# Performance work log

Measured on AMD Instinct MI355X. Metric: run time of the kernel, lower is better.

Reference implementation:

```python
import jax, jax.numpy as jnp
import numpy as np

EMBED_DIM = 1024
NUM_HEADS = 16
HEAD_DIM = EMBED_DIM // NUM_HEADS
SCALE = HEAD_DIM ** -0.5


def setup_inputs() -> dict:
    key = jax.random.key(0)
    k_x, k_wqkv, k_bqkv, k_wo, k_bo = jax.random.split(key, 5)
    B, T, C = 2, 2048, EMBED_DIM
    bound = 1.0 / np.sqrt(C)
    return {
        "x": jax.random.normal(k_x, (B, T, C), dtype=jnp.float32),
        "w_qkv": jax.random.uniform(k_wqkv, (C, 3 * C), jnp.float32, -bound, bound),
        "b_qkv": jax.random.uniform(k_bqkv, (3 * C,), jnp.float32, -bound, bound),
        "w_out": jax.random.uniform(k_wo, (C, C), jnp.float32, -bound, bound),
        "b_out": jax.random.uniform(k_bo, (C,), jnp.float32, -bound, bound),
    }


def reference(x, w_qkv, b_qkv, w_out, b_out):
    B, T, C = x.shape
    H, D = NUM_HEADS, HEAD_DIM
    qkv = x @ w_qkv + b_qkv                      # [B,T,3C]
    q, k, v = jnp.split(qkv, 3, axis=-1)         # each [B,T,C]
    q = q.reshape(B, T, H, D).transpose(0, 2, 1, 3)  # [B,H,T,D]
    k = k.reshape(B, T, H, D).transpose(0, 2, 1, 3)
    v = v.reshape(B, T, H, D).transpose(0, 2, 1, 3)
    scores = jnp.einsum("bhqd,bhkd->bhqk", q, k) * SCALE  # [B,H,T,T]
    weights = jax.nn.softmax(scores, axis=-1)
    out = jnp.einsum("bhqk,bhkd->bhqd", weights, v)       # [B,H,T,D]
    concat = out.transpose(0, 2, 1, 3).reshape(B, T, C)
    return concat @ w_out + b_out
```

## Files before the change

kernel.cpp:

```cpp
#include <hip/hip_runtime.h>

typedef _Float16 f16;
typedef _Float16 f16x8 __attribute__((ext_vector_type(8)));
typedef _Float16 f16x4 __attribute__((ext_vector_type(4)));
typedef float f32x4 __attribute__((ext_vector_type(4)));
typedef float f32x16 __attribute__((ext_vector_type(16)));
typedef unsigned int u32x4 __attribute__((ext_vector_type(4)));

#define SCALE_Q (0.125f * 1.44269504088896f)

__device__ __forceinline__ f32x4 mfma16x16x32(f16x8 a, f16x8 b, f32x4 c) {
  return __builtin_amdgcn_mfma_f32_16x16x32_f16(a, b, c, 0, 0, 0);
}
__device__ __forceinline__ f32x16 mfma32x32x16(f16x8 a, f16x8 b, f32x16 c) {
  return __builtin_amdgcn_mfma_f32_32x32x16_f16(a, b, c, 0, 0, 0);
}

__device__ __forceinline__ float fexp2(float x) {
  return __builtin_amdgcn_exp2f(x);
}

typedef const __attribute__((address_space(1))) void* gptr1;
typedef __attribute__((address_space(3))) void* lptr3;
__device__ __forceinline__ void gload_lds16(const void* g, void* l) {
  __builtin_amdgcn_global_load_lds((gptr1)g, (lptr3)l, 16, 0, 0);
}

__device__ __forceinline__ unsigned pk2(float a, float b) {
  return __builtin_bit_cast(unsigned, __builtin_amdgcn_cvt_pkrtz(a, b));
}

__global__ __launch_bounds__(256)
void prep(const float* __restrict__ x, f16* __restrict__ xh,
          const float* __restrict__ w_qkv, f16* __restrict__ wqkvT,
          const float* __restrict__ w_out, f16* __restrict__ woutT) {
  __shared__ float tile[32][33];
  const int bid = blockIdx.x;
  const int tid = threadIdx.x;
  if (bid < 4096) {
    int i = bid * 256 + tid;
    float4 v = reinterpret_cast<const float4*>(x)[i];
    f16x4 o = {(f16)v.x, (f16)v.y, (f16)v.z, (f16)v.w};
    reinterpret_cast<f16x4*>(xh)[i] = o;
    return;
  }
  const float* in;
  f16* out;
  int bx, by, R, Cin;
  if (bid < 7168) {
    int t = bid - 4096;
    in = w_qkv; out = wqkvT; R = 1024; Cin = 3072;
    bx = (t % 96) * 32; by = (t / 96) * 32;
  } else {
    int t = bid - 7168;
    in = w_out; out = woutT; R = 1024; Cin = 1024;
    bx = (t % 32) * 32; by = (t / 32) * 32;
  }
  int tx = tid & 31, ty = tid >> 5;
#pragma unroll
  for (int i = ty; i < 32; i += 8)
    tile[i][tx] = in[(size_t)(by + i) * Cin + bx + tx];
  __syncthreads();
#pragma unroll
  for (int i = ty; i < 32; i += 8)
    out[(size_t)(bx + i) * R + by + tx] = (f16)tile[tx][i];
}

__global__ __launch_bounds__(256)
void gemm_qkv(const f16* __restrict__ A, const f16* __restrict__ Bt,
              const float* __restrict__ bias, f16* __restrict__ qQ,
              f16* __restrict__ kP, f16* __restrict__ vP) {
  constexpr int BM = 128, BN = 128, BK = 32, K = 1024;
  __shared__ f16 As[BM * BK];
  __shared__ f16 Bs[BN * BK];
  const int tid = threadIdx.x;
  const int l = tid & 63;
  const int w = tid >> 6;
  const int wr = w >> 1, wc = w & 1;
  const int bid = blockIdx.x;
  const int xcd = bid & 7, idx = bid >> 3;
  const int xg = xcd & 3, yg = xcd >> 2;
  const int mx = xg * 8 + (idx & 7);
  const int ny = yg * 12 + (idx >> 3);
  const int bm = mx * BM, bn = ny * BN;
  const int l15 = l & 15, lhi = l >> 4;

  f32x4 acc[4][4] = {};

  const char* Ab = (const char*)A;
  const char* Bb = (const char*)Bt;
  const size_t rowbytes = (size_t)K * 2;

  for (int kt = 0; kt < K; kt += BK) {
    __syncthreads();
#pragma unroll
    for (int c = 0; c < 2; ++c) {
      int o = tid * 16 + c * 4096;
      int r = o >> 6;
      int cb = o & 63;
      gload_lds16(Ab + (size_t)(bm + r) * rowbytes + (size_t)kt * 2 + cb, (char*)As + o);
      gload_lds16(Bb + (size_t)(bn + r) * rowbytes + (size_t)kt * 2 + cb, (char*)Bs + o);
    }
    __syncthreads();

    f16x8 af[4], bf[4];
#pragma unroll
    for (int i = 0; i < 4; ++i)
      af[i] = *reinterpret_cast<const f16x8*>(&As[(wr * 64 + i * 16 + l15) * BK + 8 * lhi]);
#pragma unroll
    for (int i = 0; i < 4; ++i)
      bf[i] = *reinterpret_cast<const f16x8*>(&Bs[(wc * 64 + i * 16 + l15) * BK + 8 * lhi]);
#pragma unroll
    for (int i = 0; i < 4; ++i)
#pragma unroll
      for (int j = 0; j < 4; ++j)
        acc[i][j] = mfma16x16x32(af[i], bf[j], acc[i][j]);
  }

  const int region = bn >> 10;
#pragma unroll
  for (int i = 0; i < 4; ++i) {
#pragma unroll
    for (int j = 0; j < 4; ++j) {
      int gr0 = bm + wr * 64 + i * 16 + 4 * lhi;
      int gc = bn + wc * 64 + j * 16 + l15;
      float bia = bias[gc];
      if (region == 0) {
#pragma unroll
        for (int r = 0; r < 4; ++r) {
          float v = (acc[i][j][r] + bia) * SCALE_Q;
          qQ[(size_t)(gr0 + r) * 1024 + gc] = (f16)v;
        }
      } else if (region == 1) {
        int dloc = gc - 1024;
        int h = dloc >> 6, dd = dloc & 63;
        int kd = dd >> 4, hi8 = (dd >> 3) & 1, j8 = dd & 7;
        int bb = gr0 >> 11;
        int pair = bb * 16 + h;
#pragma unroll
        for (int r = 0; r < 4; ++r) {
          int key = (gr0 + r) & 2047;
          int t32 = key >> 5, l31k = key & 31;
          size_t idxp = ((((size_t)pair * 64 + t32) * 4 + kd) * 64 + (hi8 * 32 + l31k)) * 8 + j8;
          kP[idxp] = (f16)(acc[i][j][r] + bia);
        }
      } else {
        int dloc = gc - 2048;
        int h = dloc >> 6, dd = dloc & 63;
        int dhalf = dd >> 5, l31v = dd & 31;
        int bb = gr0 >> 11;
        int pair = bb * 16 + h;
        int key = gr0 & 2047;
        int t64 = key >> 6;
        int k6 = key & 63;
        int ks = k6 >> 4, hiv = (k6 >> 3) & 1, jv = k6 & 7;
        int rr = dhalf * 4 + ks;
        size_t idxp = ((((size_t)pair * 32 + t64) * 8 + rr) * 64 + (hiv * 32 + l31v)) * 8 + jv;
        f16x4 ov;
#pragma unroll
        for (int r = 0; r < 4; ++r) ov[r] = (f16)(acc[i][j][r] + bia);
        *reinterpret_cast<f16x4*>(&vP[idxp]) = ov;
      }
    }
  }
}

__global__ __launch_bounds__(256)
void gemm_out(const f16* __restrict__ A, const f16* __restrict__ Bt,
              const float* __restrict__ bias, float* __restrict__ outf) {
  constexpr int BM = 128, BN = 128, BK = 32, K = 1024, N = 1024;
  __shared__ f16 As[BM * BK];
  __shared__ f16 Bs[BN * BK];
  const int tid = threadIdx.x;
  const int l = tid & 63;
  const int w = tid >> 6;
  const int wr = w >> 1, wc = w & 1;
  const int bid = blockIdx.x;
  const int xcd = bid & 7, idx = bid >> 3;
  const int mx = xcd * 4 + (idx & 3);
  const int ny = idx >> 2;
  const int bm = mx * BM, bn = ny * BN;
  const int l15 = l & 15, lhi = l >> 4;

  f32x4 acc[4][4] = {};

  const char* Ab = (const char*)A;
  const char* Bb = (const char*)Bt;
  const size_t rowbytes = (size_t)K * 2;

  for (int kt = 0; kt < K; kt += BK) {
    __syncthreads();
#pragma unroll
    for (int c = 0; c < 2; ++c) {
      int o = tid * 16 + c * 4096;
      int r = o >> 6;
      int cb = o & 63;
      gload_lds16(Ab + (size_t)(bm + r) * rowbytes + (size_t)kt * 2 + cb, (char*)As + o);
      gload_lds16(Bb + (size_t)(bn + r) * rowbytes + (size_t)kt * 2 + cb, (char*)Bs + o);
    }
    __syncthreads();

    f16x8 af[4], bf[4];
#pragma unroll
    for (int i = 0; i < 4; ++i)
      af[i] = *reinterpret_cast<const f16x8*>(&As[(wr * 64 + i * 16 + l15) * BK + 8 * lhi]);
#pragma unroll
    for (int i = 0; i < 4; ++i)
      bf[i] = *reinterpret_cast<const f16x8*>(&Bs[(wc * 64 + i * 16 + l15) * BK + 8 * lhi]);
#pragma unroll
    for (int i = 0; i < 4; ++i)
#pragma unroll
      for (int j = 0; j < 4; ++j)
        acc[i][j] = mfma16x16x32(af[i], bf[j], acc[i][j]);
  }

#pragma unroll
  for (int i = 0; i < 4; ++i) {
#pragma unroll
    for (int j = 0; j < 4; ++j) {
      int gr0 = bm + wr * 64 + i * 16 + 4 * lhi;
      int gc = bn + wc * 64 + j * 16 + l15;
      float b = bias[gc];
#pragma unroll
      for (int r = 0; r < 4; ++r)
        outf[(size_t)(gr0 + r) * N + gc] = acc[i][j][r] + b;
    }
  }
}

__global__ __launch_bounds__(256, 3)
void attn_kernel(const f16* __restrict__ qQ, const f16* __restrict__ kP,
                 const f16* __restrict__ vP, f16* __restrict__ outh) {
  constexpr int T = 2048;
  __shared__ float mo[4096];
  __shared__ float MlBuf[2][64];

  const int tid = threadIdx.x;
  const int l = tid & 63;
  const int w = tid >> 6;
  const int wq = w >> 1;
  const int grp = w & 1;
  const int l31 = l & 31, hi = l >> 5;

  const int bid = blockIdx.x;
  const int pair = bid & 31;
  const int b = pair >> 4;
  const int h = pair & 15;
  const int qt = bid >> 5;

  const int q0 = qt * 64 + wq * 32;

  f16x8 bq[4];
  {
    const f16* qp = qQ + (size_t)(b * T + q0 + l31) * 1024 + h * 64 + hi * 8;
#pragma unroll
    for (int kd = 0; kd < 4; ++kd)
      bq[kd] = *reinterpret_cast<const f16x8*>(qp + kd * 16);
  }

  const f16* Kp = kP + (size_t)pair * 131072;
  const f16* Vp = vP + (size_t)pair * 131072;

  f32x16 o0 = {}, o1 = {};
  float l_r = 0.f;

  for (int t = 0; t < 16; ++t) {
    const int t64g = grp * 16 + t;
    const int t32g = t64g * 2;

    f16x8 ak[2][4];
#pragma unroll
    for (int kt = 0; kt < 2; ++kt)
#pragma unroll
      for (int kd = 0; kd < 4; ++kd)
        ak[kt][kd] = *reinterpret_cast<const f16x8*>(
            Kp + ((((size_t)t32g + kt) * 4 + kd) * 64 + l) * 8);

    f16x8 av0[4], av1[4];
#pragma unroll
    for (int ks = 0; ks < 4; ++ks) {
      av0[ks] = *reinterpret_cast<const f16x8*>(
          Vp + (((size_t)t64g * 8 + ks) * 64 + l) * 8);
      av1[ks] = *reinterpret_cast<const f16x8*>(
          Vp + (((size_t)t64g * 8 + 4 + ks) * 64 + l) * 8);
    }

    f32x16 s0 = {}, s1 = {};
    __builtin_amdgcn_s_setprio(1);
#pragma unroll
    for (int kd = 0; kd < 4; ++kd) s0 = mfma32x32x16(ak[0][kd], bq[kd], s0);
#pragma unroll
    for (int kd = 0; kd < 4; ++kd) s1 = mfma32x32x16(ak[1][kd], bq[kd], s1);
    __builtin_amdgcn_s_setprio(0);

    float sm[16];
#pragma unroll
    for (int r = 0; r < 16; ++r) {
      s0[r] = fexp2(s0[r]);
      s1[r] = fexp2(s1[r]);
      sm[r] = s0[r] + s1[r];
    }
#pragma unroll
    for (int st = 8; st > 0; st >>= 1)
#pragma unroll
      for (int r = 0; r < st; ++r) sm[r] += sm[r + st];
    l_r += sm[0] + __shfl_xor(sm[0], 32);

    f16x8 bp[4];
#pragma unroll
    for (int kt = 0; kt < 2; ++kt) {
#pragma unroll
      for (int s2 = 0; s2 < 2; ++s2) {
        u32x4 wd;
#pragma unroll
        for (int u = 0; u < 2; ++u) {
          float a0 = kt ? s1[8 * s2 + 2 * u] : s0[8 * s2 + 2 * u];
          float a1 = kt ? s1[8 * s2 + 2 * u + 1] : s0[8 * s2 + 2 * u + 1];
          float b0 = kt ? s1[8 * s2 + 4 + 2 * u] : s0[8 * s2 + 4 + 2 * u];
          float b1 = kt ? s1[8 * s2 + 4 + 2 * u + 1] : s0[8 * s2 + 4 + 2 * u + 1];
          unsigned wB = pk2(a0, a1);
          unsigned wA = pk2(b0, b1);
          unsigned oB = __shfl_xor(wB, 32);
          unsigned oA = __shfl_xor(wA, 32);
          wd[u]     = hi ? oA : wB;
          wd[2 + u] = hi ? wA : oB;
        }
        bp[2 * kt + s2] = __builtin_bit_cast(f16x8, wd);
      }
    }

    __builtin_amdgcn_s_setprio(1);
#pragma unroll
    for (int ks = 0; ks < 4; ++ks) {
      o0 = mfma32x32x16(av0[ks], bp[ks], o0);
      o1 = mfma32x32x16(av1[ks], bp[ks], o1);
    }
    __builtin_amdgcn_s_setprio(0);
  }

  const int mbase = wq * 2048 + l * 32;
  if (grp == 1) {
#pragma unroll
    for (int k = 0; k < 8; ++k) {
      int ks = k ^ (l & 7);
      f32x4 v;
      if (k < 4) { v = f32x4{o0[4*k], o0[4*k+1], o0[4*k+2], o0[4*k+3]}; }
      else       { int r = 4*(k-4); v = f32x4{o1[r], o1[r+1], o1[r+2], o1[r+3]}; }
      *reinterpret_cast<f32x4*>(&mo[mbase + ks * 4]) = v;
    }
    MlBuf[wq][l] = l_r;
  }
  __syncthreads();
  if (grp == 0) {
    float inv = 1.0f / (l_r + MlBuf[wq][l]);
    f16* orow = outh + (size_t)(b * T + q0 + l31) * 1024 + h * 64;
#pragma unroll
    for (int k = 0; k < 8; ++k) {
      int ks = k ^ (l & 7);
      f32x4 ob = *reinterpret_cast<const f32x4*>(&mo[mbase + ks * 4]);
#pragma unroll
      for (int j = 0; j < 4; ++j) {
        int r = 4 * (k & 3) + j;
        int d = (r & 3) + 8 * (r >> 2) + 4 * hi;
        float own = (k < 4) ? o0[r] : o1[r];
        float val = (own + ob[j]) * inv;
        orow[(k < 4 ? d : d + 32)] = (f16)val;
      }
    }
  }
}

extern "C" void kernel_launch(void* const* d_in, const int* in_sizes, int n_in,
                              void* d_out, int out_size, void* d_ws, size_t ws_size,
                              hipStream_t stream) {
  const float* x      = (const float*)d_in[0];
  const float* w_qkv  = (const float*)d_in[1];
  const float* b_qkv  = (const float*)d_in[2];
  const float* w_out  = (const float*)d_in[3];
  const float* b_out  = (const float*)d_in[4];
  float* out = (float*)d_out;

  char* ws = (char*)d_ws;
  f16* xh    = (f16*)(ws);
  f16* wqkvT = (f16*)(ws + 8388608);
  f16* woutT = (f16*)(ws + 14680064);
  f16* qQ    = (f16*)(ws + 16777216);
  f16* kP    = (f16*)(ws + 25165824);
  f16* vP    = (f16*)(ws + 33554432);
  f16* attnh = (f16*)(ws + 41943040);

  prep<<<8192, 256, 0, stream>>>(x, xh, w_qkv, wqkvT, w_out, woutT);
  gemm_qkv<<<768, 256, 0, stream>>>(xh, wqkvT, b_qkv, qQ, kP, vP);
  attn_kernel<<<1024, 256, 0, stream>>>(qQ, kP, vP, attnh);
  gemm_out<<<256, 256, 0, stream>>>(attnh, woutT, b_out, out);
}
```

Baseline: 125.0 us.

## Double-buffer K fragments in attention and shrink out-projection tile to 128x64

The attention loop now prefetches the next K tile into a second register buffer while the current tile's softmax and PV MMAs run. It is unrolled by two with ping-pong buffers, and the occupancy hint drops from 3 to 2 blocks per CU to make room for the extra registers. Separately, the output GEMM tile changes from 128x128 to 128x64 with a 4x1 wave layout, doubling the grid to 512 blocks to fill more CUs. The risks are lower attention occupancy and a redundant K load on the final iteration.

```diff
diff --git a/kernel.cpp b/kernel.cpp
--- a/kernel.cpp
+++ b/kernel.cpp
@@ -168,13 +168,12 @@
 __global__ __launch_bounds__(256)
 void gemm_out(const f16* __restrict__ A, const f16* __restrict__ Bt,
               const float* __restrict__ bias, float* __restrict__ outf) {
-  constexpr int BM = 128, BN = 128, BK = 32, K = 1024, N = 1024;
+  constexpr int BM = 128, BN = 64, BK = 32, K = 1024, N = 1024;
   __shared__ f16 As[BM * BK];
   __shared__ f16 Bs[BN * BK];
   const int tid = threadIdx.x;
   const int l = tid & 63;
   const int w = tid >> 6;
-  const int wr = w >> 1, wc = w & 1;
   const int bid = blockIdx.x;
   const int xcd = bid & 7, idx = bid >> 3;
   const int mx = xcd * 4 + (idx & 3);
@@ -182,7 +181,7 @@
   const int bm = mx * BM, bn = ny * BN;
   const int l15 = l & 15, lhi = l >> 4;
 
-  f32x4 acc[4][4] = {};
+  f32x4 acc[2][4] = {};
 
   const char* Ab = (const char*)A;
   const char* Bb = (const char*)Bt;
@@ -196,30 +195,35 @@
       int r = o >> 6;
       int cb = o & 63;
       gload_lds16(Ab + (size_t)(bm + r) * rowbytes + (size_t)kt * 2 + cb, (char*)As + o);
+    }
+    {
+      int o = tid * 16;
+      int r = o >> 6;
+      int cb = o & 63;
       gload_lds16(Bb + (size_t)(bn + r) * rowbytes + (size_t)kt * 2 + cb, (char*)Bs + o);
     }
     __syncthreads();
 
-    f16x8 af[4], bf[4];
-#pragma unroll
-    for (int i = 0; i < 4; ++i)
-      af[i] = *reinterpret_cast<const f16x8*>(&As[(wr * 64 + i * 16 + l15) * BK + 8 * lhi]);
-#pragma unroll
-    for (int i = 0; i < 4; ++i)
-      bf[i] = *reinterpret_cast<const f16x8*>(&Bs[(wc * 64 + i * 16 + l15) * BK + 8 * lhi]);
-#pragma unroll
-    for (int i = 0; i < 4; ++i)
+    f16x8 af[2], bf[4];
+#pragma unroll
+    for (int i = 0; i < 2; ++i)
+      af[i] = *reinterpret_cast<const f16x8*>(&As[(w * 32 + i * 16 + l15) * BK + 8 * lhi]);
+#pragma unroll
+    for (int j = 0; j < 4; ++j)
+      bf[j] = *reinterpret_cast<const f16x8*>(&Bs[(j * 16 + l15) * BK + 8 * lhi]);
+#pragma unroll
+    for (int i = 0; i < 2; ++i)
 #pragma unroll
       for (int j = 0; j < 4; ++j)
         acc[i][j] = mfma16x16x32(af[i], bf[j], acc[i][j]);
   }
 
 #pragma unroll
-  for (int i = 0; i < 4; ++i) {
+  for (int i = 0; i < 2; ++i) {
 #pragma unroll
     for (int j = 0; j < 4; ++j) {
-      int gr0 = bm + wr * 64 + i * 16 + 4 * lhi;
-      int gc = bn + wc * 64 + j * 16 + l15;
+      int gr0 = bm + w * 32 + i * 16 + 4 * lhi;
+      int gc = bn + j * 16 + l15;
       float b = bias[gc];
 #pragma unroll
       for (int r = 0; r < 4; ++r)
@@ -228,7 +232,7 @@
   }
 }
 
-__global__ __launch_bounds__(256, 3)
+__global__ __launch_bounds__(256, 2)
 void attn_kernel(const f16* __restrict__ qQ, const f16* __restrict__ kP,
                  const f16* __restrict__ vP, f16* __restrict__ outh) {
   constexpr int T = 2048;
@@ -263,79 +267,78 @@
 
   f32x16 o0 = {}, o1 = {};
   float l_r = 0.f;
-
-  for (int t = 0; t < 16; ++t) {
-    const int t64g = grp * 16 + t;
-    const int t32g = t64g * 2;
-
-    f16x8 ak[2][4];
-#pragma unroll
-    for (int kt = 0; kt < 2; ++kt)
-#pragma unroll
-      for (int kd = 0; kd < 4; ++kd)
-        ak[kt][kd] = *reinterpret_cast<const f16x8*>(
-            Kp + ((((size_t)t32g + kt) * 4 + kd) * 64 + l) * 8);
-
-    f16x8 av0[4], av1[4];
-#pragma unroll
-    for (int ks = 0; ks < 4; ++ks) {
-      av0[ks] = *reinterpret_cast<const f16x8*>(
-          Vp + (((size_t)t64g * 8 + ks) * 64 + l) * 8);
-      av1[ks] = *reinterpret_cast<const f16x8*>(
-          Vp + (((size_t)t64g * 8 + 4 + ks) * 64 + l) * 8);
-    }
-
-    f32x16 s0 = {}, s1 = {};
-    __builtin_amdgcn_s_setprio(1);
-#pragma unroll
-    for (int kd = 0; kd < 4; ++kd) s0 = mfma32x32x16(ak[0][kd], bq[kd], s0);
-#pragma unroll
-    for (int kd = 0; kd < 4; ++kd) s1 = mfma32x32x16(ak[1][kd], bq[kd], s1);
-    __builtin_amdgcn_s_setprio(0);
-
-    float sm[16];
-#pragma unroll
-    for (int r = 0; r < 16; ++r) {
-      s0[r] = fexp2(s0[r]);
-      s1[r] = fexp2(s1[r]);
-      sm[r] = s0[r] + s1[r];
-    }
-#pragma unroll
-    for (int st = 8; st > 0; st >>= 1)
-#pragma unroll
-      for (int r = 0; r < st; ++r) sm[r] += sm[r + st];
-    l_r += sm[0] + __shfl_xor(sm[0], 32);
-
-    f16x8 bp[4];
-#pragma unroll
-    for (int kt = 0; kt < 2; ++kt) {
-#pragma unroll
-      for (int s2 = 0; s2 < 2; ++s2) {
-        u32x4 wd;
-#pragma unroll
-        for (int u = 0; u < 2; ++u) {
-          float a0 = kt ? s1[8 * s2 + 2 * u] : s0[8 * s2 + 2 * u];
-          float a1 = kt ? s1[8 * s2 + 2 * u + 1] : s0[8 * s2 + 2 * u + 1];
-          float b0 = kt ? s1[8 * s2 + 4 + 2 * u] : s0[8 * s2 + 4 + 2 * u];
-          float b1 = kt ? s1[8 * s2 + 4 + 2 * u + 1] : s0[8 * s2 + 4 + 2 * u + 1];
-          unsigned wB = pk2(a0, a1);
-          unsigned wA = pk2(b0, b1);
-          unsigned oB = __shfl_xor(wB, 32);
-          unsigned oA = __shfl_xor(wA, 32);
-          wd[u]     = hi ? oA : wB;
-          wd[2 + u] = hi ? wA : oB;
-        }
-        bp[2 * kt + s2] = __builtin_bit_cast(f16x8, wd);
-      }
-    }
-
-    __builtin_amdgcn_s_setprio(1);
-#pragma unroll
-    for (int ks = 0; ks < 4; ++ks) {
-      o0 = mfma32x32x16(av0[ks], bp[ks], o0);
-      o1 = mfma32x32x16(av1[ks], bp[ks], o1);
-    }
-    __builtin_amdgcn_s_setprio(0);
+  const int tbase = grp * 16;
+
+#define LOADK_TO(AK, T64)                                                      \
+  do {                                                                         \
+    _Pragma("unroll") for (int kt = 0; kt < 2; ++kt)                           \
+    _Pragma("unroll") for (int kd = 0; kd < 4; ++kd)                           \
+      AK[kt][kd] = *reinterpret_cast<const f16x8*>(                            \
+          Kp + ((((size_t)(T64) * 2 + kt) * 4 + kd) * 64 + l) * 8);            \
+  } while (0)
+
+#define TILE_BODY(AKC, AKN, TT, TN)                                            \
+  do {                                                                         \
+    const int t64g = tbase + (TT);                                             \
+                         \
+    f16x8 av0[4], av1[4];                                                      \
+    _Pragma("unroll") for (int ks = 0; ks < 4; ++ks) {                         \
+      av0[ks] = *reinterpret_cast<const f16x8*>(                               \
+          Vp + (((size_t)t64g * 8 + ks) * 64 + l) * 8);                        \
+      av1[ks] = *reinterpret_cast<const f16x8*>(                               \
+          Vp + (((size_t)t64g * 8 + 4 + ks) * 64 + l) * 8);                    \
+    }                                                                          \
+    f32x16 s0 = {}, s1 = {};                                                   \
+    __builtin_amdgcn_s_setprio(1);                                             \
+    _Pragma("unroll") for (int kd = 0; kd < 4; ++kd)                           \
+      s0 = mfma32x32x16(AKC[0][kd], bq[kd], s0);                               \
+    _Pragma("unroll") for (int kd = 0; kd < 4; ++kd)                           \
+      s1 = mfma32x32x16(AKC[1][kd], bq[kd], s1);                               \
+    __builtin_amdgcn_s_setprio(0);                                             \
+      \
+    LOADK_TO(AKN, tbase + (TN));                                               \
+    float sm[16];                                                              \
+    _Pragma("unroll") for (int r = 0; r < 16; ++r) {                           \
+      s0[r] = fexp2(s0[r]);                                                    \
+      s1[r] = fexp2(s1[r]);                                                    \
+      sm[r] = s0[r] + s1[r];                                                   \
+    }                                                                          \
+    _Pragma("unroll") for (int st = 8; st > 0; st >>= 1)                       \
+      _Pragma("unroll") for (int r = 0; r < st; ++r) sm[r] += sm[r + st];      \
+    l_r += sm[0] + __shfl_xor(sm[0], 32);                                      \
+    f16x8 bp[4];                                                               \
+    _Pragma("unroll") for (int kt = 0; kt < 2; ++kt) {                         \
+      _Pragma("unroll") for (int s2 = 0; s2 < 2; ++s2) {                       \
+        u32x4 wd;                                                              \
+        _Pragma("unroll") for (int u = 0; u < 2; ++u) {                        \
+          float a0 = kt ? s1[8 * s2 + 2 * u] : s0[8 * s2 + 2 * u];             \
+          float a1 = kt ? s1[8 * s2 + 2 * u + 1] : s0[8 * s2 + 2 * u + 1];     \
+          float b0 = kt ? s1[8 * s2 + 4 + 2 * u] : s0[8 * s2 + 4 + 2 * u];     \
+          float b1 = kt ? s1[8 * s2 + 4 + 2 * u + 1] : s0[8 * s2 + 4 + 2 * u + 1]; \
+          unsigned wB = pk2(a0, a1);                                           \
+          unsigned wA = pk2(b0, b1);                                           \
+          unsigned oB = __shfl_xor(wB, 32);                                    \
+          unsigned oA = __shfl_xor(wA, 32);                                    \
+          wd[u]     = hi ? oA : wB;                                            \
+          wd[2 + u] = hi ? wA : oB;                                            \
+        }                                                                      \
+        bp[2 * kt + s2] = __builtin_bit_cast(f16x8, wd);                       \
+      }                                                                        \
+    }                                                                          \
+    __builtin_amdgcn_s_setprio(1);                                             \
+    _Pragma("unroll") for (int ks = 0; ks < 4; ++ks) {                         \
+      o0 = mfma32x32x16(av0[ks], bp[ks], o0);                                  \
+      o1 = mfma32x32x16(av1[ks], bp[ks], o1);                                  \
+    }                                                                          \
+    __builtin_amdgcn_s_setprio(0);                                             \
+  } while (0)
+
+  f16x8 akA[2][4], akB[2][4];
+  LOADK_TO(akA, tbase);
+#pragma unroll 1
+  for (int t = 0; t < 16; t += 2) {
+    TILE_BODY(akA, akB, t, t + 1);
+    TILE_BODY(akB, akA, t + 1, (t + 2 < 16 ? t + 2 : 15));
   }
 
   const int mbase = wq * 2048 + l * 32;
@@ -368,6 +371,8 @@
       }
     }
   }
+#undef LOADK_TO
+#undef TILE_BODY
 }
 
 extern "C" void kernel_launch(void* const* d_in, const int* in_sizes, int n_in,
@@ -392,5 +397,5 @@
   prep<<<8192, 256, 0, stream>>>(x, xh, w_qkv, wqkvT, w_out, woutT);
   gemm_qkv<<<768, 256, 0, stream>>>(xh, wqkvT, b_qkv, qQ, kP, vP);
   attn_kernel<<<1024, 256, 0, stream>>>(qQ, kP, vP, attnh);
-  gemm_out<<<256, 256, 0, stream>>>(attnh, woutT, b_out, out);
-}
+  gemm_out<<<512, 256, 0, stream>>>(attnh, woutT, b_out, out);
+}
```

Measured after the change: 119.9 us. 4.1% less time.
